# Performance work log

Measured on AMD Instinct MI355X. Metric: run time of the kernel, lower is better.

Reference implementation:

```python
import jax, jax.numpy as jnp
import numpy as np

EMB = 384
RANK = 8


def feature2token(f):
    # [B,C,H,W] -> [B,HW,C]
    B, C, H, W = f.shape
    return f.reshape(B, C, H * W).transpose(0, 2, 1)


def token2feature(t, H, W):
    # [B,N,C] -> [B,C,H,W]
    B, N, C = t.shape
    return t.transpose(0, 2, 1).reshape(B, C, H, W)


def linear(t, w, b):
    # torch Linear: y = t @ w.T + b ; w: [out,in]
    return jnp.einsum('bnc,oc->bno', t, w) + b


def hard_mask(y_soft, k):
    # straight-through one-hot mask of the top-k entries of y_soft, per row
    B, N = y_soft.shape
    idx = jax.lax.top_k(y_soft, k)[1]                      # [B,k]
    y_hard = jnp.zeros_like(y_soft).at[jnp.arange(B)[:, None], idx].set(1.0)
    return y_hard - jax.lax.stop_gradient(y_soft) + y_soft


def gumbel_masks(scores, k):
    # scores: [B,N] raw logits; module applies log_softmax then softmax
    y_soft = jax.nn.softmax(jax.nn.log_softmax(scores, axis=-1), axis=-1)
    token_mask = hard_mask(y_soft, k)        # top-k
    rej_mask = hard_mask(-y_soft, k) + 2.0 * jax.lax.stop_gradient(y_soft) - 2.0 * y_soft
    # note: rej uses topk of (-y_soft) for indices but straight-through around +y_soft,
    # so compute it directly for clarity:
    B, N = y_soft.shape
    idx_bot = jax.lax.top_k(-y_soft, k)[1]
    y_hard_bot = jnp.zeros_like(y_soft).at[jnp.arange(B)[:, None], idx_bot].set(1.0)
    rej_mask = y_hard_bot - jax.lax.stop_gradient(y_soft) + y_soft
    return token_mask, rej_mask


def setup_inputs() -> dict:
    key = jax.random.key(0)
    ks = jax.random.split(key, 20)
    B, C, H, W = 32, EMB, 32, 32
    s_emb = 1.0 / np.sqrt(EMB)
    s_2r = 1.0 / np.sqrt(2 * RANK)
    s_r = 1.0 / np.sqrt(RANK)
    inp = {
        'x': jax.random.normal(ks[0], (B, 2 * C, H, W), jnp.float32),
        'gx_w': jax.random.uniform(ks[1], (1, EMB), jnp.float32, -s_emb, s_emb),
        'gx_b': jax.random.uniform(ks[2], (1,), jnp.float32, -s_emb, s_emb),
        'gm_w': jax.random.uniform(ks[3], (1, EMB), jnp.float32, -s_emb, s_emb),
        'gm_b': jax.random.uniform(ks[4], (1,), jnp.float32, -s_emb, s_emb),
        'px_w': jax.random.uniform(ks[5], (RANK, EMB), jnp.float32, -s_emb, s_emb),
        'px_b': jax.random.uniform(ks[6], (RANK,), jnp.float32, -s_emb, s_emb),
        'pm_w': jax.random.uniform(ks[7], (RANK, EMB), jnp.float32, -s_emb, s_emb),
        'pm_b': jax.random.uniform(ks[8], (RANK,), jnp.float32, -s_emb, s_emb),
        'prx_w': jax.random.uniform(ks[9], (RANK, EMB), jnp.float32, -s_emb, s_emb),
        'prx_b': jax.random.uniform(ks[10], (RANK,), jnp.float32, -s_emb, s_emb),
        'prm_w': jax.random.uniform(ks[11], (RANK, EMB), jnp.float32, -s_emb, s_emb),
        'prm_b': jax.random.uniform(ks[12], (RANK,), jnp.float32, -s_emb, s_emb),
        'pfx_w': jax.random.uniform(ks[13], (RANK, 2 * RANK), jnp.float32, -s_2r, s_2r),
        'pfx_b': jax.random.uniform(ks[14], (RANK,), jnp.float32, -s_2r, s_2r),
        'pfm_w': jax.random.uniform(ks[15], (RANK, 2 * RANK), jnp.float32, -s_2r, s_2r),
        'pfm_b': jax.random.uniform(ks[16], (RANK,), jnp.float32, -s_2r, s_2r),
        'pb_w': jax.random.uniform(ks[17], (EMB, RANK), jnp.float32, -s_r, s_r),
        'pb_b': jax.random.uniform(ks[18], (EMB,), jnp.float32, -s_r, s_r),
    }
    return inp


def reference(x, gx_w, gx_b, gm_w, gm_b, px_w, px_b, pm_w, pm_b,
              prx_w, prx_b, prm_w, prm_b, pfx_w, pfx_b, pfm_w, pfm_b,
              pb_w, pb_b):
    xh, modh = jnp.split(x, 2, axis=1)           # each [B,C,H,W]
    H, W = xh.shape[2], xh.shape[3]
    xt = feature2token(xh)                        # [B,N,C]
    mt = feature2token(modh)
    B, N, _ = xt.shape
    k = N // 4

    # x-branch
    scores_x = linear(xt, gx_w, gx_b).reshape(B, N)
    tm_x, rm_x = gumbel_masks(scores_x, k)
    tm_x, rm_x = tm_x[..., None], rm_x[..., None]             # [B,N,1] broadcast over emb
    low_x = linear(xt * tm_x + mt * rm_x, px_w, px_b)
    low_res_x = linear((xt + mt) * (1.0 - rm_x - tm_x), prx_w, prx_b)
    fuse_x = linear(jnp.concatenate([low_x, low_res_x], axis=2), pfx_w, pfx_b)

    # mod-branch
    scores_m = linear(mt, gm_w, gm_b).reshape(B, N)
    tm_m, rm_m = gumbel_masks(scores_m, k)
    tm_m, rm_m = tm_m[..., None], rm_m[..., None]
    low_m = linear(mt * tm_m + xt * rm_m, pm_w, pm_b)
    low_res_m = linear((xt + mt) * (1.0 - rm_m - tm_m), prm_w, prm_b)
    fuse_m = linear(jnp.concatenate([low_m, low_res_m], axis=2), pfm_w, pfm_b)

    fuse = linear(fuse_x + fuse_m, pb_w, pb_b)   # [B,N,EMB]
    return token2feature(fuse, H, W)
```

## Files before the change

### kernel.cpp

```cpp
#include <hip/hip_runtime.h>

#define NTOK 1024
#define KSEL 256


template <int CS>
__global__ __launch_bounds__(128) void k1_proj(
    const float* __restrict__ x,
    const float* __restrict__ gx_w, const float* __restrict__ gm_w,
    const float* __restrict__ px_w, const float* __restrict__ pm_w,
    const float* __restrict__ prx_w, const float* __restrict__ prm_w,
    float* __restrict__ Pp)
{
  constexpr int NS = 384 / CS;
  constexpr int SB = (NS == 1) ? 0 : 2;
  int blk = blockIdx.x;
  int part = blk & 1;
  int ntile = (blk >> 1) & 7;
  int s = (blk >> 4) & (NS - 1);
  int b = blk >> (4 + SB);
  int n = ntile * 128 + threadIdx.x;
  const float* gw = part ? gm_w : gx_w;
  int cw0 = s * CS;

  float acc[33];
  #pragma unroll
  for (int j = 0; j < 33; ++j) acc[j] = 0.f;

  const float* xp = x + ((size_t)b * 768 + part * 384 + cw0) * NTOK + n;
  #pragma unroll 8
  for (int c = 0; c < CS; ++c) {
    float v = xp[(size_t)c * NTOK];
    int cw = cw0 + c;
    acc[0] = fmaf(gw[cw], v, acc[0]);
    #pragma unroll
    for (int r = 0; r < 8; ++r) {
      acc[1 + r]  = fmaf(px_w[r * 384 + cw],  v, acc[1 + r]);
      acc[9 + r]  = fmaf(pm_w[r * 384 + cw],  v, acc[9 + r]);
      acc[17 + r] = fmaf(prx_w[r * 384 + cw], v, acc[17 + r]);
      acc[25 + r] = fmaf(prm_w[r * 384 + cw], v, acc[25 + r]);
    }
  }
  float* op = Pp + ((((size_t)s * 32 + b) * 2 + part) * 33) * NTOK + n;
  #pragma unroll
  for (int j = 0; j < 33; ++j) op[(size_t)j * NTOK] = acc[j];
}

__global__ __launch_bounds__(64) void k2_masks(
    const float* __restrict__ Ppart, float* __restrict__ masks, int nsplit)
{
  int b = blockIdx.x >> 1;
  int branch = blockIdx.x & 1;
  int lane = threadIdx.x;
  unsigned long long lmask = (1ull << lane) - 1ull;

  float v[16];
  #pragma unroll
  for (int i = 0; i < 16; ++i) v[i] = 0.f;
  for (int s = 0; s < nsplit; ++s) {
    const float* sp = Ppart + (((size_t)s * 32 + b) * 2 + branch) * 33 * NTOK;
    #pragma unroll
    for (int i = 0; i < 16; ++i) v[i] += sp[i * 64 + lane];
  }
  unsigned key[16];
  #pragma unroll
  for (int i = 0; i < 16; ++i) {
    float f = v[i] + 0.0f;
    unsigned bits = __float_as_uint(f);
    key[i] = (bits & 0x80000000u) ? ~bits : (bits | 0x80000000u);
  }

  for (int which = 0; which < 2; ++which) {
    unsigned prefix = 0u;
    for (int bit = 31; bit >= 0; --bit) {
      unsigned cand = prefix | (1u << bit);
      int cnt = 0;
      #pragma unroll
      for (int i = 0; i < 16; ++i) {
        unsigned kk = which ? ~key[i] : key[i];
        cnt += __popcll(__ballot(kk >= cand));
      }
      if (cnt >= KSEL) prefix = cand;
    }
    int cgt = 0;
    #pragma unroll
    for (int i = 0; i < 16; ++i) {
      unsigned kk = which ? ~key[i] : key[i];
      cgt += __popcll(__ballot(kk > prefix));
    }
    int quota = KSEL - cgt;
    float* mp = masks + ((size_t)b * 4 + branch * 2 + which) * NTOK;
    int run = 0;
    #pragma unroll
    for (int i = 0; i < 16; ++i) {
      unsigned kk = which ? ~key[i] : key[i];
      bool eq = (kk == prefix);
      unsigned long long bal = __ballot(eq);
      int rank = run + __popcll(bal & lmask);
      bool sel = (kk > prefix) || (eq && rank < quota);
      mp[i * 64 + lane] = sel ? 1.0f : 0.0f;
      run += __popcll(bal);
    }
  }
}

template <int NS>
__global__ __launch_bounds__(256) void k3_g(
    const float* __restrict__ Ppart, const float* __restrict__ masks,
    const float* __restrict__ px_b, const float* __restrict__ pm_b,
    const float* __restrict__ prx_b, const float* __restrict__ prm_b,
    const float* __restrict__ pfx_w, const float* __restrict__ pfx_b,
    const float* __restrict__ pfm_w, const float* __restrict__ pfm_b,
    float* __restrict__ G)
{
  int idx = blockIdx.x * 256 + threadIdx.x;
  int b = idx >> 10;
  int n = idx & 1023;

  float ax[8], am[8], bxv[8], bmv[8], cx[8], cm[8];
  #pragma unroll
  for (int r = 0; r < 8; ++r) {
    ax[r] = am[r] = bxv[r] = bmv[r] = cx[r] = cm[r] = 0.f;
  }
  #pragma unroll
  for (int s = 0; s < NS; ++s) {
    const float* P0 = Ppart + (((size_t)s * 32 + b) * 2 + 0) * 33 * NTOK + n;
    const float* P1 = Ppart + (((size_t)s * 32 + b) * 2 + 1) * 33 * NTOK + n;
    #pragma unroll
    for (int r = 0; r < 8; ++r) {
      ax[r]  += P0[(size_t)(1 + r) * NTOK];
      am[r]  += P1[(size_t)(1 + r) * NTOK];
      bmv[r] += P0[(size_t)(9 + r) * NTOK];
      bxv[r] += P1[(size_t)(9 + r) * NTOK];
      cx[r]  += P0[(size_t)(17 + r) * NTOK] + P1[(size_t)(17 + r) * NTOK];
      cm[r]  += P0[(size_t)(25 + r) * NTOK] + P1[(size_t)(25 + r) * NTOK];
    }
  }
  const float* mk = masks + (size_t)b * 4 * NTOK + n;
  float tmx = mk[0 * NTOK], rmx = mk[1 * NTOK];
  float tmm = mk[2 * NTOK], rmm = mk[3 * NTOK];
  float wx = 1.0f - tmx - rmx;
  float wm = 1.0f - tmm - rmm;

  float lowx[8], lrx[8], lowm[8], lrm[8];
  #pragma unroll
  for (int r = 0; r < 8; ++r) {
    lowx[r] = fmaf(tmx, ax[r], fmaf(rmx, am[r], px_b[r]));
    lrx[r]  = fmaf(wx, cx[r], prx_b[r]);
    lowm[r] = fmaf(tmm, bxv[r], fmaf(rmm, bmv[r], pm_b[r]));
    lrm[r]  = fmaf(wm, cm[r], prm_b[r]);
  }
  float g[8];
  #pragma unroll
  for (int r = 0; r < 8; ++r) {
    float acc = pfx_b[r] + pfm_b[r];
    #pragma unroll
    for (int s2 = 0; s2 < 8; ++s2) {
      acc = fmaf(pfx_w[r * 16 + s2],     lowx[s2], acc);
      acc = fmaf(pfx_w[r * 16 + 8 + s2], lrx[s2],  acc);
      acc = fmaf(pfm_w[r * 16 + s2],     lowm[s2], acc);
      acc = fmaf(pfm_w[r * 16 + 8 + s2], lrm[s2],  acc);
    }
    g[r] = acc;
  }
  float4* Gp = reinterpret_cast<float4*>(G + ((size_t)b * NTOK + n) * 8);
  Gp[0] = make_float4(g[0], g[1], g[2], g[3]);
  Gp[1] = make_float4(g[4], g[5], g[6], g[7]);
}

__global__ __launch_bounds__(128) void k4_out(
    const float* __restrict__ G, const float* __restrict__ pb_w,
    const float* __restrict__ pb_b, float* __restrict__ out)
{
  int blk = blockIdx.x;
  int cpart = blk & 3;
  int ntile = (blk >> 2) & 7;
  int b = blk >> 5;
  int n = ntile * 128 + threadIdx.x;

  const float4* Gp = reinterpret_cast<const float4*>(G + ((size_t)b * NTOK + n) * 8);
  float4 g0 = Gp[0], g1 = Gp[1];

  float* op = out + ((size_t)b * 384 + (size_t)cpart * 96) * NTOK + n;
  const float* wp = pb_w + (size_t)cpart * 96 * 8;
  const float* bp = pb_b + (size_t)cpart * 96;
  #pragma unroll 4
  for (int c = 0; c < 96; ++c) {
    const float* w = wp + c * 8;
    float acc = bp[c];
    acc = fmaf(w[0], g0.x, acc);
    acc = fmaf(w[1], g0.y, acc);
    acc = fmaf(w[2], g0.z, acc);
    acc = fmaf(w[3], g0.w, acc);
    acc = fmaf(w[4], g1.x, acc);
    acc = fmaf(w[5], g1.y, acc);
    acc = fmaf(w[6], g1.z, acc);
    acc = fmaf(w[7], g1.w, acc);
    op[(size_t)c * NTOK] = acc;
  }
}

extern "C" void kernel_launch(void* const* d_in, const int* in_sizes, int n_in,
                              void* d_out, int out_size, void* d_ws, size_t ws_size,
                              hipStream_t stream) {
  const float* x     = (const float*)d_in[0];
  const float* gx_w  = (const float*)d_in[1];
  const float* gm_w  = (const float*)d_in[3];
  const float* px_w  = (const float*)d_in[5];
  const float* px_b  = (const float*)d_in[6];
  const float* pm_w  = (const float*)d_in[7];
  const float* pm_b  = (const float*)d_in[8];
  const float* prx_w = (const float*)d_in[9];
  const float* prx_b = (const float*)d_in[10];
  const float* prm_w = (const float*)d_in[11];
  const float* prm_b = (const float*)d_in[12];
  const float* pfx_w = (const float*)d_in[13];
  const float* pfx_b = (const float*)d_in[14];
  const float* pfm_w = (const float*)d_in[15];
  const float* pfm_b = (const float*)d_in[16];
  const float* pb_w  = (const float*)d_in[17];
  const float* pb_b  = (const float*)d_in[18];
  float* out = (float*)d_out;

  const size_t P1_F   = 32ull * 2 * 33 * NTOK;
  const size_t MASK_F = 32ull * 4 * NTOK;
  const size_t G_F    = 32ull * NTOK * 8;
  const size_t need4  = (4 * P1_F + MASK_F + G_F) * 4;

  float* ws = (float*)d_ws;
  if (ws_size >= need4) {
    float* Ppart = ws;
    float* masks = ws + 4 * P1_F;
    float* G     = masks + MASK_F;
    k1_proj<96><<<2048, 128, 0, stream>>>(x, gx_w, gm_w, px_w, pm_w, prx_w, prm_w, Ppart);
    k2_masks<<<64, 64, 0, stream>>>(Ppart, masks, 4);
    k3_g<4><<<128, 256, 0, stream>>>(Ppart, masks, px_b, pm_b, prx_b, prm_b,
                                     pfx_w, pfx_b, pfm_w, pfm_b, G);
    k4_out<<<1024, 128, 0, stream>>>(G, pb_w, pb_b, out);
  } else {
    float* Ppart = ws;
    float* masks = ws + P1_F;
    float* G     = masks + MASK_F;
    k1_proj<384><<<512, 128, 0, stream>>>(x, gx_w, gm_w, px_w, pm_w, prx_w, prm_w, Ppart);
    k2_masks<<<64, 64, 0, stream>>>(Ppart, masks, 1);
    k3_g<1><<<128, 256, 0, stream>>>(Ppart, masks, px_b, pm_b, prx_b, prm_b,
                                     pfx_w, pfx_b, pfm_w, pfm_b, G);
    k4_out<<<1024, 128, 0, stream>>>(G, pb_w, pb_b, out);
  }
}
```

Measured before the change: 306.7 us.

## Split low-rank stage into two kernels, prefetch input in k1, vectorize output stores

The projection kernel now double-buffers 16-channel blocks of the input so loads for the next block are issued before the FMAs on the current one. The old k3_g, which ran on only 128 blocks, is split into k3a (one block per batch and rank, 256 blocks of 1024 threads) and k3b, with intermediate low-rank values staged through a new workspace buffer. k4_out now computes four tokens per thread and writes float4 stores, using fewer threads. The changes aim to hide load latency and raise parallelism in the small middle stage, at the cost of an extra launch, extra global traffic for the staged buffer, and higher register pressure in k1.

Measured after the change: 300.2 us. 2.1% less time.

```diff
diff --git a/kernel.cpp b/kernel.cpp
--- a/kernel.cpp
+++ b/kernel.cpp
@@ -14,6 +14,7 @@
 {
   constexpr int NS = 384 / CS;
   constexpr int SB = (NS == 1) ? 0 : 2;
+  constexpr int NCB = CS / 16;
   int blk = blockIdx.x;
   int part = blk & 1;
   int ntile = (blk >> 1) & 7;
@@ -28,18 +29,31 @@
   for (int j = 0; j < 33; ++j) acc[j] = 0.f;
 
   const float* xp = x + ((size_t)b * 768 + part * 384 + cw0) * NTOK + n;
-  #pragma unroll 8
-  for (int c = 0; c < CS; ++c) {
-    float v = xp[(size_t)c * NTOK];
-    int cw = cw0 + c;
-    acc[0] = fmaf(gw[cw], v, acc[0]);
-    #pragma unroll
-    for (int r = 0; r < 8; ++r) {
-      acc[1 + r]  = fmaf(px_w[r * 384 + cw],  v, acc[1 + r]);
-      acc[9 + r]  = fmaf(pm_w[r * 384 + cw],  v, acc[9 + r]);
-      acc[17 + r] = fmaf(prx_w[r * 384 + cw], v, acc[17 + r]);
-      acc[25 + r] = fmaf(prm_w[r * 384 + cw], v, acc[25 + r]);
-    }
+
+  float cur[16], nxt[16];
+  #pragma unroll
+  for (int i = 0; i < 16; ++i) cur[i] = xp[(size_t)i * NTOK];
+
+  #pragma unroll
+  for (int cb = 0; cb < NCB; ++cb) {
+    #pragma unroll
+    for (int i = 0; i < 16; ++i)
+      nxt[i] = (cb + 1 < NCB) ? xp[(size_t)((cb + 1) * 16 + i) * NTOK] : 0.f;
+    #pragma unroll
+    for (int i = 0; i < 16; ++i) {
+      int cw = cw0 + cb * 16 + i;
+      float v = cur[i];
+      acc[0] = fmaf(gw[cw], v, acc[0]);
+      #pragma unroll
+      for (int r = 0; r < 8; ++r) {
+        acc[1 + r]  = fmaf(px_w[r * 384 + cw],  v, acc[1 + r]);
+        acc[9 + r]  = fmaf(pm_w[r * 384 + cw],  v, acc[9 + r]);
+        acc[17 + r] = fmaf(prx_w[r * 384 + cw], v, acc[17 + r]);
+        acc[25 + r] = fmaf(prm_w[r * 384 + cw], v, acc[25 + r]);
+      }
+    }
+    #pragma unroll
+    for (int i = 0; i < 16; ++i) cur[i] = nxt[i];
   }
   float* op = Pp + ((((size_t)s * 32 + b) * 2 + part) * 33) * NTOK + n;
   #pragma unroll
@@ -105,36 +119,27 @@
 }
 
 template <int NS>
-__global__ __launch_bounds__(256) void k3_g(
+__global__ __launch_bounds__(1024) void k3a(
     const float* __restrict__ Ppart, const float* __restrict__ masks,
     const float* __restrict__ px_b, const float* __restrict__ pm_b,
     const float* __restrict__ prx_b, const float* __restrict__ prm_b,
-    const float* __restrict__ pfx_w, const float* __restrict__ pfx_b,
-    const float* __restrict__ pfm_w, const float* __restrict__ pfm_b,
-    float* __restrict__ G)
-{
-  int idx = blockIdx.x * 256 + threadIdx.x;
-  int b = idx >> 10;
-  int n = idx & 1023;
-
-  float ax[8], am[8], bxv[8], bmv[8], cx[8], cm[8];
-  #pragma unroll
-  for (int r = 0; r < 8; ++r) {
-    ax[r] = am[r] = bxv[r] = bmv[r] = cx[r] = cm[r] = 0.f;
-  }
+    float* __restrict__ LOWS)
+{
+  int r = blockIdx.x & 7;
+  int b = blockIdx.x >> 3;
+  int n = threadIdx.x;
+
+  float ax = 0.f, am = 0.f, bmv = 0.f, bxv = 0.f, cx = 0.f, cm = 0.f;
   #pragma unroll
   for (int s = 0; s < NS; ++s) {
     const float* P0 = Ppart + (((size_t)s * 32 + b) * 2 + 0) * 33 * NTOK + n;
     const float* P1 = Ppart + (((size_t)s * 32 + b) * 2 + 1) * 33 * NTOK + n;
-    #pragma unroll
-    for (int r = 0; r < 8; ++r) {
-      ax[r]  += P0[(size_t)(1 + r) * NTOK];
-      am[r]  += P1[(size_t)(1 + r) * NTOK];
-      bmv[r] += P0[(size_t)(9 + r) * NTOK];
-      bxv[r] += P1[(size_t)(9 + r) * NTOK];
-      cx[r]  += P0[(size_t)(17 + r) * NTOK] + P1[(size_t)(17 + r) * NTOK];
-      cm[r]  += P0[(size_t)(25 + r) * NTOK] + P1[(size_t)(25 + r) * NTOK];
-    }
+    ax  += P0[(size_t)(1 + r) * NTOK];
+    am  += P1[(size_t)(1 + r) * NTOK];
+    bmv += P0[(size_t)(9 + r) * NTOK];
+    bxv += P1[(size_t)(9 + r) * NTOK];
+    cx  += P0[(size_t)(17 + r) * NTOK] + P1[(size_t)(17 + r) * NTOK];
+    cm  += P0[(size_t)(25 + r) * NTOK] + P1[(size_t)(25 + r) * NTOK];
   }
   const float* mk = masks + (size_t)b * 4 * NTOK + n;
   float tmx = mk[0 * NTOK], rmx = mk[1 * NTOK];
@@ -142,13 +147,34 @@
   float wx = 1.0f - tmx - rmx;
   float wm = 1.0f - tmm - rmm;
 
+  float lowx = fmaf(tmx, ax, fmaf(rmx, am, px_b[r]));
+  float lrx  = fmaf(wx, cx, prx_b[r]);
+  float lowm = fmaf(tmm, bxv, fmaf(rmm, bmv, pm_b[r]));
+  float lrm  = fmaf(wm, cm, prm_b[r]);
+
+  float* L = LOWS + ((size_t)b * 32 + r) * NTOK + n;
+  L[0 * 8 * NTOK] = lowx;
+  L[1 * 8 * NTOK] = lrx;
+  L[2 * 8 * NTOK] = lowm;
+  L[3 * 8 * NTOK] = lrm;
+}
+
+__global__ __launch_bounds__(1024) void k3b(
+    const float* __restrict__ LOWS,
+    const float* __restrict__ pfx_w, const float* __restrict__ pfx_b,
+    const float* __restrict__ pfm_w, const float* __restrict__ pfm_b,
+    float* __restrict__ G)
+{
+  int b = blockIdx.x;
+  int n = threadIdx.x;
+  const float* L = LOWS + (size_t)b * 32 * NTOK + n;
   float lowx[8], lrx[8], lowm[8], lrm[8];
   #pragma unroll
   for (int r = 0; r < 8; ++r) {
-    lowx[r] = fmaf(tmx, ax[r], fmaf(rmx, am[r], px_b[r]));
-    lrx[r]  = fmaf(wx, cx[r], prx_b[r]);
-    lowm[r] = fmaf(tmm, bxv[r], fmaf(rmm, bmv[r], pm_b[r]));
-    lrm[r]  = fmaf(wm, cm[r], prm_b[r]);
+    lowx[r] = L[(size_t)(0 * 8 + r) * NTOK];
+    lrx[r]  = L[(size_t)(1 * 8 + r) * NTOK];
+    lowm[r] = L[(size_t)(2 * 8 + r) * NTOK];
+    lrm[r]  = L[(size_t)(3 * 8 + r) * NTOK];
   }
   float g[8];
   #pragma unroll
@@ -168,35 +194,50 @@
   Gp[1] = make_float4(g[4], g[5], g[6], g[7]);
 }
 
-__global__ __launch_bounds__(128) void k4_out(
+__global__ __launch_bounds__(64) void k4_out(
     const float* __restrict__ G, const float* __restrict__ pb_w,
     const float* __restrict__ pb_b, float* __restrict__ out)
 {
   int blk = blockIdx.x;
-  int cpart = blk & 3;
-  int ntile = (blk >> 2) & 7;
-  int b = blk >> 5;
-  int n = ntile * 128 + threadIdx.x;
-
-  const float4* Gp = reinterpret_cast<const float4*>(G + ((size_t)b * NTOK + n) * 8);
-  float4 g0 = Gp[0], g1 = Gp[1];
-
-  float* op = out + ((size_t)b * 384 + (size_t)cpart * 96) * NTOK + n;
+  int ttile = blk & 3;
+  int cpart = (blk >> 2) & 3;
+  int b = blk >> 4;
+  int n0 = ttile * 256 + threadIdx.x * 4;
+
+  const float4* Gp = reinterpret_cast<const float4*>(G + ((size_t)b * NTOK + n0) * 8);
+  float4 ga0 = Gp[0], ga1 = Gp[1];
+  float4 gb0 = Gp[2], gb1 = Gp[3];
+  float4 gc0 = Gp[4], gc1 = Gp[5];
+  float4 gd0 = Gp[6], gd1 = Gp[7];
+
+  float* op = out + ((size_t)b * 384 + (size_t)cpart * 96) * NTOK + n0;
   const float* wp = pb_w + (size_t)cpart * 96 * 8;
   const float* bp = pb_b + (size_t)cpart * 96;
   #pragma unroll 4
   for (int c = 0; c < 96; ++c) {
     const float* w = wp + c * 8;
-    float acc = bp[c];
-    acc = fmaf(w[0], g0.x, acc);
-    acc = fmaf(w[1], g0.y, acc);
-    acc = fmaf(w[2], g0.z, acc);
-    acc = fmaf(w[3], g0.w, acc);
-    acc = fmaf(w[4], g1.x, acc);
-    acc = fmaf(w[5], g1.y, acc);
-    acc = fmaf(w[6], g1.z, acc);
-    acc = fmaf(w[7], g1.w, acc);
-    op[(size_t)c * NTOK] = acc;
+    float w0 = w[0], w1 = w[1], w2 = w[2], w3 = w[3];
+    float w4 = w[4], w5 = w[5], w6 = w[6], w7 = w[7];
+    float bb = bp[c];
+    float4 o;
+    o.x = bb; o.y = bb; o.z = bb; o.w = bb;
+    o.x = fmaf(w0, ga0.x, o.x); o.x = fmaf(w1, ga0.y, o.x);
+    o.x = fmaf(w2, ga0.z, o.x); o.x = fmaf(w3, ga0.w, o.x);
+    o.x = fmaf(w4, ga1.x, o.x); o.x = fmaf(w5, ga1.y, o.x);
+    o.x = fmaf(w6, ga1.z, o.x); o.x = fmaf(w7, ga1.w, o.x);
+    o.y = fmaf(w0, gb0.x, o.y); o.y = fmaf(w1, gb0.y, o.y);
+    o.y = fmaf(w2, gb0.z, o.y); o.y = fmaf(w3, gb0.w, o.y);
+    o.y = fmaf(w4, gb1.x, o.y); o.y = fmaf(w5, gb1.y, o.y);
+    o.y = fmaf(w6, gb1.z, o.y); o.y = fmaf(w7, gb1.w, o.y);
+    o.z = fmaf(w0, gc0.x, o.z); o.z = fmaf(w1, gc0.y, o.z);
+    o.z = fmaf(w2, gc0.z, o.z); o.z = fmaf(w3, gc0.w, o.z);
+    o.z = fmaf(w4, gc1.x, o.z); o.z = fmaf(w5, gc1.y, o.z);
+    o.z = fmaf(w6, gc1.z, o.z); o.z = fmaf(w7, gc1.w, o.z);
+    o.w = fmaf(w0, gd0.x, o.w); o.w = fmaf(w1, gd0.y, o.w);
+    o.w = fmaf(w2, gd0.z, o.w); o.w = fmaf(w3, gd0.w, o.w);
+    o.w = fmaf(w4, gd1.x, o.w); o.w = fmaf(w5, gd1.y, o.w);
+    o.w = fmaf(w6, gd1.z, o.w); o.w = fmaf(w7, gd1.w, o.w);
+    *reinterpret_cast<float4*>(op + (size_t)c * NTOK) = o;
   }
 }
 
@@ -225,26 +266,29 @@
   const size_t P1_F   = 32ull * 2 * 33 * NTOK;
   const size_t MASK_F = 32ull * 4 * NTOK;
   const size_t G_F    = 32ull * NTOK * 8;
-  const size_t need4  = (4 * P1_F + MASK_F + G_F) * 4;
+  const size_t LOWS_F = 32ull * 32 * NTOK;
+  const size_t need4  = (4 * P1_F + MASK_F + G_F + LOWS_F) * 4;
 
   float* ws = (float*)d_ws;
   if (ws_size >= need4) {
     float* Ppart = ws;
     float* masks = ws + 4 * P1_F;
     float* G     = masks + MASK_F;
+    float* LOWS  = G + G_F;
     k1_proj<96><<<2048, 128, 0, stream>>>(x, gx_w, gm_w, px_w, pm_w, prx_w, prm_w, Ppart);
     k2_masks<<<64, 64, 0, stream>>>(Ppart, masks, 4);
-    k3_g<4><<<128, 256, 0, stream>>>(Ppart, masks, px_b, pm_b, prx_b, prm_b,
-                                     pfx_w, pfx_b, pfm_w, pfm_b, G);
-    k4_out<<<1024, 128, 0, stream>>>(G, pb_w, pb_b, out);
+    k3a<4><<<256, 1024, 0, stream>>>(Ppart, masks, px_b, pm_b, prx_b, prm_b, LOWS);
+    k3b<<<32, 1024, 0, stream>>>(LOWS, pfx_w, pfx_b, pfm_w, pfm_b, G);
+    k4_out<<<512, 64, 0, stream>>>(G, pb_w, pb_b, out);
   } else {
     float* Ppart = ws;
     float* masks = ws + P1_F;
     float* G     = masks + MASK_F;
+    float* LOWS  = G + G_F;
     k1_proj<384><<<512, 128, 0, stream>>>(x, gx_w, gm_w, px_w, pm_w, prx_w, prm_w, Ppart);
     k2_masks<<<64, 64, 0, stream>>>(Ppart, masks, 1);
-    k3_g<1><<<128, 256, 0, stream>>>(Ppart, masks, px_b, pm_b, prx_b, prm_b,
-                                     pfx_w, pfx_b, pfm_w, pfm_b, G);
-    k4_out<<<1024, 128, 0, stream>>>(G, pb_w, pb_b, out);
-  }
-}
+    k3a<1><<<256, 1024, 0, stream>>>(Ppart, masks, px_b, pm_b, prx_b, prm_b, LOWS);
+    k3b<<<32, 1024, 0, stream>>>(LOWS, pfx_w, pfx_b, pfm_w, pfm_b, G);
+    k4_out<<<512, 64, 0, stream>>>(G, pb_w, pb_b, out);
+  }
+}
```

## Fuse rank-mix and output projection kernels; process two tokens per thread in projection

Applied to the files above, without the earlier changes.

The projection kernel now handles two adjacent tokens per thread using float2 loads and stores, halving the grid and reusing each weight load across two FMAs. The separate G-computation and output-expansion kernels are merged into one kernel that stages the low-rank values and the mixed 8-vector in shared memory, then writes the 384-channel output directly. This removes the G workspace round trip and one launch, and spreads the partial-sum reduction across four thread groups. The costs are higher register pressure in the projection kernel, fewer blocks there, and two block-level barriers in the fused kernel.

Result: faster. 274.8 us (-10.4%).

```diff
diff --git a/kernel.cpp b/kernel.cpp
--- a/kernel.cpp
+++ b/kernel.cpp
@@ -4,7 +4,7 @@
 #define KSEL 256
 
 
-template <int CS>
+template <int NS>
 __global__ __launch_bounds__(128) void k1_proj(
     const float* __restrict__ x,
     const float* __restrict__ gx_w, const float* __restrict__ gm_w,
@@ -12,38 +12,49 @@
     const float* __restrict__ prx_w, const float* __restrict__ prm_w,
     float* __restrict__ Pp)
 {
-  constexpr int NS = 384 / CS;
-  constexpr int SB = (NS == 1) ? 0 : 2;
+  constexpr int CS = 384 / NS;
+  constexpr int SB = (NS == 8) ? 3 : (NS == 4) ? 2 : 0;
   int blk = blockIdx.x;
   int part = blk & 1;
-  int ntile = (blk >> 1) & 7;
-  int s = (blk >> 4) & (NS - 1);
-  int b = blk >> (4 + SB);
-  int n = ntile * 128 + threadIdx.x;
+  int ntile = (blk >> 1) & 3;
+  int s = (blk >> 3) & (NS - 1);
+  int b = blk >> (3 + SB);
+  int n0 = ntile * 256 + threadIdx.x * 2;
   const float* gw = part ? gm_w : gx_w;
   int cw0 = s * CS;
 
-  float acc[33];
-  #pragma unroll
-  for (int j = 0; j < 33; ++j) acc[j] = 0.f;
-
-  const float* xp = x + ((size_t)b * 768 + part * 384 + cw0) * NTOK + n;
+  float2 acc[33];
+  #pragma unroll
+  for (int j = 0; j < 33; ++j) { acc[j].x = 0.f; acc[j].y = 0.f; }
+
+  const float* xp = x + ((size_t)b * 768 + part * 384 + cw0) * NTOK + n0;
   #pragma unroll 8
   for (int c = 0; c < CS; ++c) {
-    float v = xp[(size_t)c * NTOK];
+    float2 v = *reinterpret_cast<const float2*>(xp + (size_t)c * NTOK);
     int cw = cw0 + c;
-    acc[0] = fmaf(gw[cw], v, acc[0]);
+    float w0 = gw[cw];
+    acc[0].x = fmaf(w0, v.x, acc[0].x);
+    acc[0].y = fmaf(w0, v.y, acc[0].y);
     #pragma unroll
     for (int r = 0; r < 8; ++r) {
-      acc[1 + r]  = fmaf(px_w[r * 384 + cw],  v, acc[1 + r]);
-      acc[9 + r]  = fmaf(pm_w[r * 384 + cw],  v, acc[9 + r]);
-      acc[17 + r] = fmaf(prx_w[r * 384 + cw], v, acc[17 + r]);
-      acc[25 + r] = fmaf(prm_w[r * 384 + cw], v, acc[25 + r]);
-    }
-  }
-  float* op = Pp + ((((size_t)s * 32 + b) * 2 + part) * 33) * NTOK + n;
-  #pragma unroll
-  for (int j = 0; j < 33; ++j) op[(size_t)j * NTOK] = acc[j];
+      float wa = px_w[r * 384 + cw];
+      float wb = pm_w[r * 384 + cw];
+      float wc = prx_w[r * 384 + cw];
+      float wd = prm_w[r * 384 + cw];
+      acc[1 + r].x  = fmaf(wa, v.x, acc[1 + r].x);
+      acc[1 + r].y  = fmaf(wa, v.y, acc[1 + r].y);
+      acc[9 + r].x  = fmaf(wb, v.x, acc[9 + r].x);
+      acc[9 + r].y  = fmaf(wb, v.y, acc[9 + r].y);
+      acc[17 + r].x = fmaf(wc, v.x, acc[17 + r].x);
+      acc[17 + r].y = fmaf(wc, v.y, acc[17 + r].y);
+      acc[25 + r].x = fmaf(wd, v.x, acc[25 + r].x);
+      acc[25 + r].y = fmaf(wd, v.y, acc[25 + r].y);
+    }
+  }
+  float* op = Pp + ((((size_t)s * 32 + b) * 2 + part) * 33) * NTOK + n0;
+  #pragma unroll
+  for (int j = 0; j < 33; ++j)
+    *reinterpret_cast<float2*>(op + (size_t)j * NTOK) = acc[j];
 }
 
 __global__ __launch_bounds__(64) void k2_masks(
@@ -105,97 +116,89 @@
 }
 
 template <int NS>
-__global__ __launch_bounds__(256) void k3_g(
+__global__ __launch_bounds__(256) void k3f(
     const float* __restrict__ Ppart, const float* __restrict__ masks,
     const float* __restrict__ px_b, const float* __restrict__ pm_b,
     const float* __restrict__ prx_b, const float* __restrict__ prm_b,
     const float* __restrict__ pfx_w, const float* __restrict__ pfx_b,
     const float* __restrict__ pfm_w, const float* __restrict__ pfm_b,
-    float* __restrict__ G)
+    const float* __restrict__ pb_w, const float* __restrict__ pb_b,
+    float* __restrict__ out)
 {
-  int idx = blockIdx.x * 256 + threadIdx.x;
-  int b = idx >> 10;
-  int n = idx & 1023;
-
-  float ax[8], am[8], bxv[8], bmv[8], cx[8], cm[8];
+  __shared__ float lows[32][64];
+  __shared__ float gl[8][64];
+  int tile = blockIdx.x & 15;
+  int b = blockIdx.x >> 4;
+  int t = threadIdx.x;
+  int tok = t & 63;
+  int kind = t >> 6;
+  int n = tile * 64 + tok;
+
+  int branch = kind >> 1;
+  const float* mk = masks + ((size_t)b * 4 + branch * 2) * NTOK + n;
+  float tm = mk[0];
+  float rm = mk[NTOK];
+  int rowbase = (kind == 0) ? 1 : (kind == 1) ? 17 : (kind == 2) ? 9 : 25;
+
   #pragma unroll
   for (int r = 0; r < 8; ++r) {
-    ax[r] = am[r] = bxv[r] = bmv[r] = cx[r] = cm[r] = 0.f;
-  }
-  #pragma unroll
-  for (int s = 0; s < NS; ++s) {
-    const float* P0 = Ppart + (((size_t)s * 32 + b) * 2 + 0) * 33 * NTOK + n;
-    const float* P1 = Ppart + (((size_t)s * 32 + b) * 2 + 1) * 33 * NTOK + n;
+    float s0 = 0.f, s1 = 0.f;
+    #pragma unroll
+    for (int sp = 0; sp < NS; ++sp) {
+      const float* P0 = Ppart + (((size_t)sp * 32 + b) * 2 + 0) * 33 * NTOK + n;
+      const float* P1 = Ppart + (((size_t)sp * 32 + b) * 2 + 1) * 33 * NTOK + n;
+      s0 += P0[(size_t)(rowbase + r) * NTOK];
+      s1 += P1[(size_t)(rowbase + r) * NTOK];
+    }
+    float val;
+    if (kind == 0)      val = fmaf(tm, s0, fmaf(rm, s1, px_b[r]));
+    else if (kind == 2) val = fmaf(tm, s1, fmaf(rm, s0, pm_b[r]));
+    else {
+      float w = 1.0f - tm - rm;
+      val = fmaf(w, s0 + s1, (kind == 1) ? prx_b[r] : prm_b[r]);
+    }
+    lows[kind * 8 + r][tok] = val;
+  }
+  __syncthreads();
+
+  if (t < 64) {
+    float L[32];
+    #pragma unroll
+    for (int i = 0; i < 32; ++i) L[i] = lows[i][tok];
     #pragma unroll
     for (int r = 0; r < 8; ++r) {
-      ax[r]  += P0[(size_t)(1 + r) * NTOK];
-      am[r]  += P1[(size_t)(1 + r) * NTOK];
-      bmv[r] += P0[(size_t)(9 + r) * NTOK];
-      bxv[r] += P1[(size_t)(9 + r) * NTOK];
-      cx[r]  += P0[(size_t)(17 + r) * NTOK] + P1[(size_t)(17 + r) * NTOK];
-      cm[r]  += P0[(size_t)(25 + r) * NTOK] + P1[(size_t)(25 + r) * NTOK];
-    }
-  }
-  const float* mk = masks + (size_t)b * 4 * NTOK + n;
-  float tmx = mk[0 * NTOK], rmx = mk[1 * NTOK];
-  float tmm = mk[2 * NTOK], rmm = mk[3 * NTOK];
-  float wx = 1.0f - tmx - rmx;
-  float wm = 1.0f - tmm - rmm;
-
-  float lowx[8], lrx[8], lowm[8], lrm[8];
-  #pragma unroll
-  for (int r = 0; r < 8; ++r) {
-    lowx[r] = fmaf(tmx, ax[r], fmaf(rmx, am[r], px_b[r]));
-    lrx[r]  = fmaf(wx, cx[r], prx_b[r]);
-    lowm[r] = fmaf(tmm, bxv[r], fmaf(rmm, bmv[r], pm_b[r]));
-    lrm[r]  = fmaf(wm, cm[r], prm_b[r]);
-  }
+      float acc = pfx_b[r] + pfm_b[r];
+      #pragma unroll
+      for (int s2 = 0; s2 < 8; ++s2) {
+        acc = fmaf(pfx_w[r * 16 + s2],     L[s2],      acc);
+        acc = fmaf(pfx_w[r * 16 + 8 + s2], L[8 + s2],  acc);
+        acc = fmaf(pfm_w[r * 16 + s2],     L[16 + s2], acc);
+        acc = fmaf(pfm_w[r * 16 + 8 + s2], L[24 + s2], acc);
+      }
+      gl[r][tok] = acc;
+    }
+  }
+  __syncthreads();
+
   float g[8];
   #pragma unroll
-  for (int r = 0; r < 8; ++r) {
-    float acc = pfx_b[r] + pfm_b[r];
-    #pragma unroll
-    for (int s2 = 0; s2 < 8; ++s2) {
-      acc = fmaf(pfx_w[r * 16 + s2],     lowx[s2], acc);
-      acc = fmaf(pfx_w[r * 16 + 8 + s2], lrx[s2],  acc);
-      acc = fmaf(pfm_w[r * 16 + s2],     lowm[s2], acc);
-      acc = fmaf(pfm_w[r * 16 + 8 + s2], lrm[s2],  acc);
-    }
-    g[r] = acc;
-  }
-  float4* Gp = reinterpret_cast<float4*>(G + ((size_t)b * NTOK + n) * 8);
-  Gp[0] = make_float4(g[0], g[1], g[2], g[3]);
-  Gp[1] = make_float4(g[4], g[5], g[6], g[7]);
-}
-
-__global__ __launch_bounds__(128) void k4_out(
-    const float* __restrict__ G, const float* __restrict__ pb_w,
-    const float* __restrict__ pb_b, float* __restrict__ out)
-{
-  int blk = blockIdx.x;
-  int cpart = blk & 3;
-  int ntile = (blk >> 2) & 7;
-  int b = blk >> 5;
-  int n = ntile * 128 + threadIdx.x;
-
-  const float4* Gp = reinterpret_cast<const float4*>(G + ((size_t)b * NTOK + n) * 8);
-  float4 g0 = Gp[0], g1 = Gp[1];
-
-  float* op = out + ((size_t)b * 384 + (size_t)cpart * 96) * NTOK + n;
-  const float* wp = pb_w + (size_t)cpart * 96 * 8;
-  const float* bp = pb_b + (size_t)cpart * 96;
+  for (int r = 0; r < 8; ++r) g[r] = gl[r][tok];
+
+  float* op = out + ((size_t)b * 384 + (size_t)kind * 96) * NTOK + n;
+  const float* wp = pb_w + (size_t)kind * 96 * 8;
+  const float* bp = pb_b + (size_t)kind * 96;
   #pragma unroll 4
   for (int c = 0; c < 96; ++c) {
     const float* w = wp + c * 8;
     float acc = bp[c];
-    acc = fmaf(w[0], g0.x, acc);
-    acc = fmaf(w[1], g0.y, acc);
-    acc = fmaf(w[2], g0.z, acc);
-    acc = fmaf(w[3], g0.w, acc);
-    acc = fmaf(w[4], g1.x, acc);
-    acc = fmaf(w[5], g1.y, acc);
-    acc = fmaf(w[6], g1.z, acc);
-    acc = fmaf(w[7], g1.w, acc);
+    acc = fmaf(w[0], g[0], acc);
+    acc = fmaf(w[1], g[1], acc);
+    acc = fmaf(w[2], g[2], acc);
+    acc = fmaf(w[3], g[3], acc);
+    acc = fmaf(w[4], g[4], acc);
+    acc = fmaf(w[5], g[5], acc);
+    acc = fmaf(w[6], g[6], acc);
+    acc = fmaf(w[7], g[7], acc);
     op[(size_t)c * NTOK] = acc;
   }
 }
@@ -224,27 +227,22 @@
 
   const size_t P1_F   = 32ull * 2 * 33 * NTOK;
   const size_t MASK_F = 32ull * 4 * NTOK;
-  const size_t G_F    = 32ull * NTOK * 8;
-  const size_t need4  = (4 * P1_F + MASK_F + G_F) * 4;
+  const size_t need4  = (4 * P1_F + MASK_F) * 4;
 
   float* ws = (float*)d_ws;
   if (ws_size >= need4) {
     float* Ppart = ws;
     float* masks = ws + 4 * P1_F;
-    float* G     = masks + MASK_F;
-    k1_proj<96><<<2048, 128, 0, stream>>>(x, gx_w, gm_w, px_w, pm_w, prx_w, prm_w, Ppart);
+    k1_proj<4><<<1024, 128, 0, stream>>>(x, gx_w, gm_w, px_w, pm_w, prx_w, prm_w, Ppart);
     k2_masks<<<64, 64, 0, stream>>>(Ppart, masks, 4);
-    k3_g<4><<<128, 256, 0, stream>>>(Ppart, masks, px_b, pm_b, prx_b, prm_b,
-                                     pfx_w, pfx_b, pfm_w, pfm_b, G);
-    k4_out<<<1024, 128, 0, stream>>>(G, pb_w, pb_b, out);
+    k3f<4><<<512, 256, 0, stream>>>(Ppart, masks, px_b, pm_b, prx_b, prm_b,
+                                    pfx_w, pfx_b, pfm_w, pfm_b, pb_w, pb_b, out);
   } else {
     float* Ppart = ws;
     float* masks = ws + P1_F;
-    float* G     = masks + MASK_F;
-    k1_proj<384><<<512, 128, 0, stream>>>(x, gx_w, gm_w, px_w, pm_w, prx_w, prm_w, Ppart);
+    k1_proj<1><<<256, 128, 0, stream>>>(x, gx_w, gm_w, px_w, pm_w, prx_w, prm_w, Ppart);
     k2_masks<<<64, 64, 0, stream>>>(Ppart, masks, 1);
-    k3_g<1><<<128, 256, 0, stream>>>(Ppart, masks, px_b, pm_b, prx_b, prm_b,
-                                     pfx_w, pfx_b, pfm_w, pfm_b, G);
-    k4_out<<<1024, 128, 0, stream>>>(G, pb_w, pb_b, out);
-  }
-}
+    k3f<1><<<512, 256, 0, stream>>>(Ppart, masks, px_b, pm_b, prx_b, prm_b,
+                                    pfx_w, pfx_b, pfm_w, pfm_b, pb_w, pb_b, out);
+  }
+}
```
